# Optimization experiments

Hardware: AMD Instinct MI355X
Metric: run time of the kernel (lower is better)

The kernel has to match this reference:

```python
import jax, jax.numpy as jnp
import numpy as np

MU = 0.9
IN_DIM = 1024
OUT_DIM = 8192
N = 8192


def setup_inputs() -> dict:
    key = jax.random.key(0)
    ks = jax.random.split(key, 8)
    stdv = 1.0 / np.sqrt(IN_DIM)
    inp = {
        "x": jax.random.normal(ks[0], (N, IN_DIM), dtype=jnp.float32),
        "x_ctx": jax.random.normal(ks[1], (N, IN_DIM), dtype=jnp.float32),
        "labels": jax.random.randint(ks[2], (N,), 0, OUT_DIM, dtype=jnp.int64),
        # classifier: uniform(-stdv, stdv), shape [output_dim, input_dim]
        "classifier": jax.random.uniform(ks[3], (OUT_DIM, IN_DIM), dtype=jnp.float32, minval=-stdv, maxval=stdv),
        # ctx_q = Linear(input_dim, output_dim - 1)  (na_att=False)
        "ctx_q_w": jax.random.uniform(ks[4], (OUT_DIM - 1, IN_DIM), dtype=jnp.float32, minval=-stdv, maxval=stdv),
        "ctx_q_b": jnp.zeros((OUT_DIM - 1,), dtype=jnp.float32),
        # word_g = Linear(input_dim, 1)
        "word_g_w": jax.random.uniform(ks[5], (1, IN_DIM), dtype=jnp.float32, minval=-stdv, maxval=stdv),
        "word_g_b": jnp.zeros((1,), dtype=jnp.float32),
        # registered buffers, initialized to zero as in __init__
        "history_input": jnp.zeros((OUT_DIM - 1, IN_DIM), dtype=jnp.float32),
        "history_count": jnp.zeros((OUT_DIM - 1,), dtype=jnp.int64),
    }
    return inp


def reference(x, x_ctx, labels, classifier, ctx_q_w, ctx_q_b, word_g_w, word_g_b,
              history_input, history_count):
    # ---- update_history: fused segment-mean EMA (replaces python loop over classes) ----
    xs = jax.lax.stop_gradient(x)  # .clone().detach() in torch
    sums = jax.ops.segment_sum(xs, labels, num_segments=OUT_DIM)          # [C, D]
    cnts = jax.ops.segment_sum(jnp.ones((N,), xs.dtype), labels, num_segments=OUT_DIM)  # [C]
    means = sums / jnp.maximum(cnts, 1.0)[:, None]                        # per-class mean
    present = cnts[1:] > 0                                                # classes 1..C-1
    new_hist = jnp.where(present[:, None], MU * history_input + means[1:], history_input)
    new_count = history_count + present.astype(history_count.dtype)

    # ---- generate_substitute ----
    w_logits = x_ctx @ ctx_q_w.T + ctx_q_b                                # [N, C-1]
    w = jax.nn.softmax(w_logits, axis=-1)
    clamped = jnp.maximum(new_count, 1).astype(x.dtype)
    v = new_hist * (1.0 - MU) / (1.0 - jnp.power(MU, clamped))[:, None]   # bias-corrected EMA
    substitute = w @ v                                                    # [N, D]

    # ---- gated mix + classifier logits ----
    g = jax.nn.sigmoid(x @ word_g_w.T + word_g_b)                         # [N, 1]
    feat = g * x + (1.0 - g) * substitute
    logits = feat @ classifier.T                                          # [N, C]

    # ---- cross_entropy over labels >= 0 (masked mean, jit-safe) ----
    mask = labels >= 0
    logp = jax.nn.log_softmax(logits, axis=-1)
    safe_lbl = jnp.maximum(labels, 0)
    nll = -jnp.take_along_axis(logp, safe_lbl[:, None], axis=1)[:, 0]
    loss = jnp.sum(jnp.where(mask, nll, 0.0)) / jnp.maximum(jnp.sum(mask), 1).astype(nll.dtype)
    return loss, logits
```

## Files before the change

kernel.cpp:

```cpp
#include <hip/hip_runtime.h>
#include <hip/hip_bf16.h>
#include <cstddef>

typedef __hip_bfloat16 bf16;
typedef float floatx4 __attribute__((ext_vector_type(4)));
typedef short shortx8 __attribute__((ext_vector_type(8)));

#define NROWS 8192
#define INDIM 1024
#define OUTDIM 8192
#define CM1 8191

__global__ __launch_bounds__(256) void seg_acc_kernel(
    const float* __restrict__ x, const int* __restrict__ labels,
    float* __restrict__ sums, int* __restrict__ cnts) {
  int i = blockIdx.x;
  int l = labels[i];
  const float* xr = x + (size_t)i * INDIM;
  float* sr = sums + (size_t)l * INDIM;
  for (int d = threadIdx.x; d < INDIM; d += 256) atomicAdd(&sr[d], xr[d]);
  if (threadIdx.x == 0) atomicAdd(&cnts[l], 1);
}

__global__ __launch_bounds__(256) void cvt_kernel(
    const float* __restrict__ in, bf16* __restrict__ out, long n) {
  long i = (long)blockIdx.x * 256 + threadIdx.x;
  if (i < n) out[i] = __float2bfloat16(in[i]);
}

__global__ __launch_bounds__(256) void cvt_pad_kernel(
    const float* __restrict__ in, bf16* __restrict__ out, long n_in, long n_out) {
  long i = (long)blockIdx.x * 256 + threadIdx.x;
  if (i < n_out) out[i] = __float2bfloat16(i < n_in ? in[i] : 0.0f);
}

__global__ __launch_bounds__(256) void make_vt_kernel(
    const float* __restrict__ sums, const int* __restrict__ cnts,
    const float* __restrict__ hist, const int* __restrict__ hist_cnt,
    bf16* __restrict__ vT) {
  size_t idx = (size_t)blockIdx.x * 256 + threadIdx.x;
  int c = (int)(idx & (OUTDIM - 1));
  int d = (int)(idx >> 13);
  float val = 0.0f;
  if (c < CM1) {
    int cnt = cnts[c + 1];
    bool present = cnt > 0;
    float mean = sums[(size_t)(c + 1) * INDIM + d] / fmaxf((float)cnt, 1.0f);
    float h = hist[(size_t)c * INDIM + d];
    float nh = present ? (0.9f * h + mean) : h;
    int nc = hist_cnt[c] + (present ? 1 : 0);
    float clamped = (float)(nc > 1 ? nc : 1);
    float scale = 0.1f / (1.0f - powf(0.9f, clamped));
    val = nh * scale;
  }
  vT[idx] = __float2bfloat16(val);
}

__device__ __forceinline__ void store_c(float* p, float v) { *p = v; }
__device__ __forceinline__ void store_c(bf16* p, float v) { *p = __float2bfloat16(v); }

template <typename OutT>
__global__ __launch_bounds__(256) void gemm_bt_kernel(
    const bf16* __restrict__ A, const bf16* __restrict__ B, OutT* __restrict__ C,
    int K, int ldc) {
  __shared__ bf16 As[128][72];
  __shared__ bf16 Bs[128][72];
  const int t = threadIdx.x;
  const int lane = t & 63;
  const int wave = t >> 6;
  const int bm = blockIdx.y * 128;
  const int bn = blockIdx.x * 128;
  const int wm = (wave >> 1) * 64;
  const int wn = (wave & 1) * 64;

  floatx4 acc[4][4];
#pragma unroll
  for (int i = 0; i < 4; i++)
#pragma unroll
    for (int j = 0; j < 4; j++) acc[i][j] = (floatx4){0.f, 0.f, 0.f, 0.f};

  const int r = lane & 15;
  const int q = lane >> 4;

  for (int k0 = 0; k0 < K; k0 += 64) {
    __syncthreads();
#pragma unroll
    for (int i = 0; i < 4; i++) {
      int c = t + i * 256;
      int row = c >> 3;
      int col = (c & 7) << 3;
      *(uint4*)(&As[row][col]) = *(const uint4*)(A + (size_t)(bm + row) * K + k0 + col);
      *(uint4*)(&Bs[row][col]) = *(const uint4*)(B + (size_t)(bn + row) * K + k0 + col);
    }
    __syncthreads();
#pragma unroll
    for (int kk = 0; kk < 64; kk += 32) {
      shortx8 af[4], bf[4];
#pragma unroll
      for (int i = 0; i < 4; i++) {
        af[i] = *(const shortx8*)(&As[wm + i * 16 + r][kk + q * 8]);
        bf[i] = *(const shortx8*)(&Bs[wn + i * 16 + r][kk + q * 8]);
      }
#pragma unroll
      for (int i = 0; i < 4; i++)
#pragma unroll
        for (int j = 0; j < 4; j++)
          acc[i][j] = __builtin_amdgcn_mfma_f32_16x16x32_bf16(af[i], bf[j], acc[i][j], 0, 0, 0);
    }
  }

#pragma unroll
  for (int i = 0; i < 4; i++)
#pragma unroll
    for (int j = 0; j < 4; j++)
#pragma unroll
      for (int rr = 0; rr < 4; rr++) {
        int m = bm + wm + i * 16 + q * 4 + rr;
        int n = bn + wn + j * 16 + r;
        store_c(&C[(size_t)m * ldc + n], acc[i][j][rr]);
      }
}

__global__ __launch_bounds__(256) void softmax_rows_kernel(
    bf16* __restrict__ wl, const float* __restrict__ bias) {
  __shared__ float red[4];
  const int t = threadIdx.x;
  bf16* p = wl + (size_t)blockIdx.x * OUTDIM;
  float vals[32];
  float mx = -1e30f;
#pragma unroll
  for (int i = 0; i < 32; i++) {
    int col = i * 256 + t;
    float v = -1e30f;
    if (col < CM1) v = __bfloat162float(p[col]) + bias[col];
    vals[i] = v;
    mx = fmaxf(mx, v);
  }
  for (int o = 32; o; o >>= 1) mx = fmaxf(mx, __shfl_down(mx, o, 64));
  if ((t & 63) == 0) red[t >> 6] = mx;
  __syncthreads();
  mx = fmaxf(fmaxf(red[0], red[1]), fmaxf(red[2], red[3]));
  __syncthreads();
  float s = 0.f;
#pragma unroll
  for (int i = 0; i < 32; i++) {
    int col = i * 256 + t;
    float e = (col < CM1) ? __expf(vals[i] - mx) : 0.f;
    vals[i] = e;
    s += e;
  }
  for (int o = 32; o; o >>= 1) s += __shfl_down(s, o, 64);
  if ((t & 63) == 0) red[t >> 6] = s;
  __syncthreads();
  s = red[0] + red[1] + red[2] + red[3];
  float rs = 1.0f / s;
#pragma unroll
  for (int i = 0; i < 32; i++) {
    int col = i * 256 + t;
    p[col] = __float2bfloat16(vals[i] * rs);
  }
}

__global__ __launch_bounds__(256) void g_feat_kernel(
    const float* __restrict__ x, const float* __restrict__ wg,
    const float* __restrict__ wgb, const bf16* __restrict__ sub,
    bf16* __restrict__ feat) {
  __shared__ float red[4];
  const int t = threadIdx.x;
  const float* xr = x + (size_t)blockIdx.x * INDIM;
  float dot = 0.f;
#pragma unroll
  for (int i = 0; i < 4; i++) {
    int d = i * 256 + t;
    dot += xr[d] * wg[d];
  }
  for (int o = 32; o; o >>= 1) dot += __shfl_down(dot, o, 64);
  if ((t & 63) == 0) red[t >> 6] = dot;
  __syncthreads();
  dot = red[0] + red[1] + red[2] + red[3];
  float g = 1.0f / (1.0f + __expf(-(dot + wgb[0])));
  const bf16* sr = sub + (size_t)blockIdx.x * INDIM;
  bf16* fr = feat + (size_t)blockIdx.x * INDIM;
#pragma unroll
  for (int i = 0; i < 4; i++) {
    int d = i * 256 + t;
    float f = g * xr[d] + (1.0f - g) * __bfloat162float(sr[d]);
    fr[d] = __float2bfloat16(f);
  }
}

__global__ __launch_bounds__(256) void ce_kernel(
    const float* __restrict__ logits, const int* __restrict__ labels,
    float* __restrict__ acc) {
  __shared__ float red[4];
  const int t = threadIdx.x;
  const float* p = logits + (size_t)blockIdx.x * OUTDIM;
  float vals[32];
  float mx = -1e30f;
#pragma unroll
  for (int i = 0; i < 32; i++) {
    float v = p[i * 256 + t];
    vals[i] = v;
    mx = fmaxf(mx, v);
  }
  for (int o = 32; o; o >>= 1) mx = fmaxf(mx, __shfl_down(mx, o, 64));
  if ((t & 63) == 0) red[t >> 6] = mx;
  __syncthreads();
  mx = fmaxf(fmaxf(red[0], red[1]), fmaxf(red[2], red[3]));
  __syncthreads();
  float s = 0.f;
#pragma unroll
  for (int i = 0; i < 32; i++) s += __expf(vals[i] - mx);
  for (int o = 32; o; o >>= 1) s += __shfl_down(s, o, 64);
  if ((t & 63) == 0) red[t >> 6] = s;
  __syncthreads();
  if (t == 0) {
    s = red[0] + red[1] + red[2] + red[3];
    int l = labels[blockIdx.x];
    if (l >= 0) {
      float nll = mx + logf(s) - p[l];
      atomicAdd(&acc[0], nll);
      atomicAdd(&acc[1], 1.0f);
    }
  }
}

__global__ void finalize_kernel(const float* __restrict__ acc, float* __restrict__ out) {
  out[0] = acc[0] / fmaxf(acc[1], 1.0f);
}

extern "C" void kernel_launch(void* const* d_in, const int* in_sizes, int n_in,
                              void* d_out, int out_size, void* d_ws, size_t ws_size,
                              hipStream_t stream) {
  const float* x        = (const float*)d_in[0];
  const float* x_ctx    = (const float*)d_in[1];
  const int*   labels   = (const int*)d_in[2];
  const float* cls      = (const float*)d_in[3];
  const float* ctxq_w   = (const float*)d_in[4];
  const float* ctxq_b   = (const float*)d_in[5];
  const float* wg_w     = (const float*)d_in[6];
  const float* wg_b     = (const float*)d_in[7];
  const float* hist     = (const float*)d_in[8];
  const int*   hist_cnt = (const int*)d_in[9];
  float* out = (float*)d_out;

  char* ws = (char*)d_ws;
  float* sums   = (float*)(ws + 0);
  int*   cnts   = (int*)  (ws + 33554432);
  float* acc    = (float*)(ws + 33587200);
  bf16* xctx_bf = (bf16*) (ws + 33587456);
  bf16* wq_bf   = (bf16*) (ws + 50364672);
  bf16* cls_bf  = (bf16*) (ws + 67141888);
  bf16* vT      = (bf16*) (ws + 83919104);
  bf16* wl      = (bf16*) (ws + 100696320);
  bf16* sub_bf  = (bf16*) (ws + 234914048);
  bf16* feat_bf = (bf16*) (ws + 251691264);

  hipMemsetAsync(ws, 0, 33587456 + 256, stream);

  seg_acc_kernel<<<NROWS, 256, 0, stream>>>(x, labels, sums, cnts);
  cvt_kernel<<<32768, 256, 0, stream>>>(x_ctx, xctx_bf, (long)NROWS * INDIM);
  cvt_pad_kernel<<<32768, 256, 0, stream>>>(ctxq_w, wq_bf, (long)CM1 * INDIM,
                                            (long)OUTDIM * INDIM);
  cvt_kernel<<<32768, 256, 0, stream>>>(cls, cls_bf, (long)OUTDIM * INDIM);
  make_vt_kernel<<<32768, 256, 0, stream>>>(sums, cnts, hist, hist_cnt, vT);

  gemm_bt_kernel<bf16><<<dim3(64, 64), 256, 0, stream>>>(xctx_bf, wq_bf, wl, 1024, OUTDIM);
  softmax_rows_kernel<<<NROWS, 256, 0, stream>>>(wl, ctxq_b);
  gemm_bt_kernel<bf16><<<dim3(8, 64), 256, 0, stream>>>(wl, vT, sub_bf, OUTDIM, INDIM);
  g_feat_kernel<<<NROWS, 256, 0, stream>>>(x, wg_w, wg_b, sub_bf, feat_bf);
  gemm_bt_kernel<float><<<dim3(64, 64), 256, 0, stream>>>(feat_bf, cls_bf, out + 1, 1024, OUTDIM);
  ce_kernel<<<NROWS, 256, 0, stream>>>(out + 1, labels, acc);
  finalize_kernel<<<1, 1, 0, stream>>>(acc, out);
}
```

Measured before the change: 1.316 ms.

## Use direct-to-LDS loads with XOR swizzle, vectorize conversions, tile vT transpose

The GEMM now loads tiles with global_load_lds straight into unpadded, XOR-swizzled shared memory, and it remaps workgroup IDs so neighbouring blocks share operand tiles in cache. The fp32-to-bf16 conversion kernels now handle eight elements per thread with vector loads and stores. make_vt now transposes through a shared-memory tile, which coalesces reads of sums and hist and writes of vT, and it computes per-class scales once. Together these target GEMM load latency, LDS bank conflicts and uncoalesced memory traffic in the preprocessing kernels. The cost is more complex code, and the GEMM still uses a single LDS buffer with no prefetch of the next tile.

```diff
diff --git a/kernel.cpp b/kernel.cpp
--- a/kernel.cpp
+++ b/kernel.cpp
@@ -1,6 +1,7 @@
 #include <hip/hip_runtime.h>
 #include <hip/hip_bf16.h>
 #include <cstddef>
+#include <cstdint>
 
 typedef __hip_bfloat16 bf16;
 typedef float floatx4 __attribute__((ext_vector_type(4)));
@@ -10,6 +11,12 @@
 #define INDIM 1024
 #define OUTDIM 8192
 #define CM1 8191
+
+__device__ __forceinline__ void gload16(const void* g, void* l) {
+  __builtin_amdgcn_global_load_lds(
+      (const __attribute__((address_space(1))) void*)g,
+      (__attribute__((address_space(3))) void*)l, 16, 0, 0);
+}
 
 __global__ __launch_bounds__(256) void seg_acc_kernel(
     const float* __restrict__ x, const int* __restrict__ labels,
@@ -22,38 +29,81 @@
   if (threadIdx.x == 0) atomicAdd(&cnts[l], 1);
 }
 
-__global__ __launch_bounds__(256) void cvt_kernel(
-    const float* __restrict__ in, bf16* __restrict__ out, long n) {
-  long i = (long)blockIdx.x * 256 + threadIdx.x;
-  if (i < n) out[i] = __float2bfloat16(in[i]);
-}
-
-__global__ __launch_bounds__(256) void cvt_pad_kernel(
+__global__ __launch_bounds__(256) void cvt8_kernel(
     const float* __restrict__ in, bf16* __restrict__ out, long n_in, long n_out) {
-  long i = (long)blockIdx.x * 256 + threadIdx.x;
-  if (i < n_out) out[i] = __float2bfloat16(i < n_in ? in[i] : 0.0f);
+  long i = ((long)blockIdx.x * 256 + threadIdx.x) * 8;
+  if (i >= n_out) return;
+  shortx8 o;
+  if (i + 8 <= n_in) {
+    floatx4 a = *(const floatx4*)(in + i);
+    floatx4 b = *(const floatx4*)(in + i + 4);
+#pragma unroll
+    for (int j = 0; j < 4; j++) {
+      o[j] = __builtin_bit_cast(short, __float2bfloat16(a[j]));
+      o[j + 4] = __builtin_bit_cast(short, __float2bfloat16(b[j]));
+    }
+  } else {
+#pragma unroll
+    for (int j = 0; j < 8; j++) o[j] = 0;
+  }
+  *(shortx8*)(out + i) = o;
 }
 
 __global__ __launch_bounds__(256) void make_vt_kernel(
     const float* __restrict__ sums, const int* __restrict__ cnts,
     const float* __restrict__ hist, const int* __restrict__ hist_cnt,
     bf16* __restrict__ vT) {
-  size_t idx = (size_t)blockIdx.x * 256 + threadIdx.x;
-  int c = (int)(idx & (OUTDIM - 1));
-  int d = (int)(idx >> 13);
-  float val = 0.0f;
-  if (c < CM1) {
-    int cnt = cnts[c + 1];
-    bool present = cnt > 0;
-    float mean = sums[(size_t)(c + 1) * INDIM + d] / fmaxf((float)cnt, 1.0f);
-    float h = hist[(size_t)c * INDIM + d];
-    float nh = present ? (0.9f * h + mean) : h;
-    int nc = hist_cnt[c] + (present ? 1 : 0);
-    float clamped = (float)(nc > 1 ? nc : 1);
-    float scale = 0.1f / (1.0f - powf(0.9f, clamped));
-    val = nh * scale;
-  }
-  vT[idx] = __float2bfloat16(val);
+  __shared__ float tile[64][65];
+  __shared__ float scl[64];
+  __shared__ float rc[64];
+  __shared__ int prs[64];
+  const int t = threadIdx.x;
+  const int cb = blockIdx.x & 127;
+  const int db = blockIdx.x >> 7;
+  const int c0 = cb * 64, d0 = db * 64;
+
+  if (t < 64) {
+    int c = c0 + t;
+    float scale = 0.f, rcnt = 0.f;
+    int present = 0;
+    if (c < CM1) {
+      int cnt = cnts[c + 1];
+      present = cnt > 0;
+      rcnt = 1.0f / fmaxf((float)cnt, 1.0f);
+      int nc = hist_cnt[c] + (present ? 1 : 0);
+      float clamped = (float)(nc > 1 ? nc : 1);
+      scale = 0.1f / (1.0f - powf(0.9f, clamped));
+    }
+    scl[t] = scale;
+    rc[t] = rcnt;
+    prs[t] = present;
+  }
+  __syncthreads();
+
+  const int dl = t & 63;
+  const int cl0 = t >> 6;
+#pragma unroll
+  for (int ii = 0; ii < 16; ii++) {
+    int clc = cl0 * 16 + ii;
+    int c = c0 + clc;
+    float val = 0.f;
+    if (c < CM1) {
+      float mean = sums[(size_t)(c + 1) * INDIM + d0 + dl] * rc[clc];
+      float h = hist[(size_t)c * INDIM + d0 + dl];
+      float nh = prs[clc] ? (0.9f * h + mean) : h;
+      val = nh * scl[clc];
+    }
+    tile[clc][dl] = val;
+  }
+  __syncthreads();
+
+  const int clw = t & 63;
+  const int dl0 = t >> 6;
+#pragma unroll
+  for (int jj = 0; jj < 16; jj++) {
+    int dlc = dl0 * 16 + jj;
+    vT[(size_t)(d0 + dlc) * OUTDIM + c0 + clw] = __float2bfloat16(tile[clw][dlc]);
+  }
 }
 
 __device__ __forceinline__ void store_c(float* p, float v) { *p = v; }
@@ -63,50 +113,56 @@
 __global__ __launch_bounds__(256) void gemm_bt_kernel(
     const bf16* __restrict__ A, const bf16* __restrict__ B, OutT* __restrict__ C,
     int K, int ldc) {
-  __shared__ bf16 As[128][72];
-  __shared__ bf16 Bs[128][72];
+  __shared__ bf16 As[128 * 64];
+  __shared__ bf16 Bs[128 * 64];
   const int t = threadIdx.x;
   const int lane = t & 63;
   const int wave = t >> 6;
-  const int bm = blockIdx.y * 128;
-  const int bn = blockIdx.x * 128;
+
+  const int nwg = gridDim.x * gridDim.y;
+  const int orig = blockIdx.y * gridDim.x + blockIdx.x;
+  const int wg = (orig & 7) * (nwg >> 3) + (orig >> 3);
+  const int bm = (wg / gridDim.x) * 128;
+  const int bn = (wg % gridDim.x) * 128;
+
   const int wm = (wave >> 1) * 64;
   const int wn = (wave & 1) * 64;
-
-  floatx4 acc[4][4];
-#pragma unroll
-  for (int i = 0; i < 4; i++)
-#pragma unroll
-    for (int j = 0; j < 4; j++) acc[i][j] = (floatx4){0.f, 0.f, 0.f, 0.f};
-
   const int r = lane & 15;
   const int q = lane >> 4;
+  const int wbase = t & 192;
+
+  floatx4 acc[4][4];
+#pragma unroll
+  for (int i = 0; i < 4; i++)
+#pragma unroll
+    for (int j = 0; j < 4; j++) acc[i][j] = (floatx4){0.f, 0.f, 0.f, 0.f};
 
   for (int k0 = 0; k0 < K; k0 += 64) {
+#pragma unroll
+    for (int i = 0; i < 4; i++) {
+      int c = i * 256 + t;
+      int row = c >> 3;
+      int gc = ((c & 7) ^ (row & 7)) << 3;
+      gload16(A + (size_t)(bm + row) * K + k0 + gc, &As[(i * 256 + wbase) * 8]);
+      gload16(B + (size_t)(bn + row) * K + k0 + gc, &Bs[(i * 256 + wbase) * 8]);
+    }
     __syncthreads();
 #pragma unroll
-    for (int i = 0; i < 4; i++) {
-      int c = t + i * 256;
-      int row = c >> 3;
-      int col = (c & 7) << 3;
-      *(uint4*)(&As[row][col]) = *(const uint4*)(A + (size_t)(bm + row) * K + k0 + col);
-      *(uint4*)(&Bs[row][col]) = *(const uint4*)(B + (size_t)(bn + row) * K + k0 + col);
+    for (int kk = 0; kk < 64; kk += 32) {
+      shortx8 af[4], bfr[4];
+      const int pc = ((kk >> 3) + q) ^ (r & 7);
+#pragma unroll
+      for (int i = 0; i < 4; i++) {
+        af[i] = *(const shortx8*)(&As[(wm + i * 16 + r) * 64 + pc * 8]);
+        bfr[i] = *(const shortx8*)(&Bs[(wn + i * 16 + r) * 64 + pc * 8]);
+      }
+#pragma unroll
+      for (int i = 0; i < 4; i++)
+#pragma unroll
+        for (int j = 0; j < 4; j++)
+          acc[i][j] = __builtin_amdgcn_mfma_f32_16x16x32_bf16(af[i], bfr[j], acc[i][j], 0, 0, 0);
     }
     __syncthreads();
-#pragma unroll
-    for (int kk = 0; kk < 64; kk += 32) {
-      shortx8 af[4], bf[4];
-#pragma unroll
-      for (int i = 0; i < 4; i++) {
-        af[i] = *(const shortx8*)(&As[wm + i * 16 + r][kk + q * 8]);
-        bf[i] = *(const shortx8*)(&Bs[wn + i * 16 + r][kk + q * 8]);
-      }
-#pragma unroll
-      for (int i = 0; i < 4; i++)
-#pragma unroll
-        for (int j = 0; j < 4; j++)
-          acc[i][j] = __builtin_amdgcn_mfma_f32_16x16x32_bf16(af[i], bf[j], acc[i][j], 0, 0, 0);
-    }
   }
 
 #pragma unroll
@@ -259,11 +315,13 @@
   hipMemsetAsync(ws, 0, 33587456 + 256, stream);
 
   seg_acc_kernel<<<NROWS, 256, 0, stream>>>(x, labels, sums, cnts);
-  cvt_kernel<<<32768, 256, 0, stream>>>(x_ctx, xctx_bf, (long)NROWS * INDIM);
-  cvt_pad_kernel<<<32768, 256, 0, stream>>>(ctxq_w, wq_bf, (long)CM1 * INDIM,
-                                            (long)OUTDIM * INDIM);
-  cvt_kernel<<<32768, 256, 0, stream>>>(cls, cls_bf, (long)OUTDIM * INDIM);
-  make_vt_kernel<<<32768, 256, 0, stream>>>(sums, cnts, hist, hist_cnt, vT);
+  cvt8_kernel<<<4096, 256, 0, stream>>>(x_ctx, xctx_bf, (long)NROWS * INDIM,
+                                        (long)NROWS * INDIM);
+  cvt8_kernel<<<4096, 256, 0, stream>>>(ctxq_w, wq_bf, (long)CM1 * INDIM,
+                                        (long)OUTDIM * INDIM);
+  cvt8_kernel<<<4096, 256, 0, stream>>>(cls, cls_bf, (long)OUTDIM * INDIM,
+                                        (long)OUTDIM * INDIM);
+  make_vt_kernel<<<2048, 256, 0, stream>>>(sums, cnts, hist, hist_cnt, vT);
 
   gemm_bt_kernel<bf16><<<dim3(64, 64), 256, 0, stream>>>(xctx_bf, wq_bf, wl, 1024, OUTDIM);
   softmax_rows_kernel<<<NROWS, 256, 0, stream>>>(wl, ctxq_b);
```

Result: faster. 1.244 ms (-5.5%).
